# Performance work log

Measured on AMD Instinct MI355X. Metric: run time of the kernel, lower is better.

## Reference

```python
import jax, jax.numpy as jnp
import numpy as np

INPUT_SIZE = 1024
HIDDEN_SIZE = 2048
BATCH = 8192


def setup_inputs() -> dict:
    key = jax.random.key(0)
    k1, k2, k3, k4, k5 = jax.random.split(key, 5)
    input_tensor = jax.random.normal(k1, (BATCH, INPUT_SIZE), dtype=jnp.float32)
    h_0 = jax.random.normal(k2, (BATCH, HIDDEN_SIZE), dtype=jnp.float32)
    c_0 = jax.random.normal(k3, (BATCH, HIDDEN_SIZE), dtype=jnp.float32)
    # parameters: weight [input_size, 3*hidden], weight_hidden [hidden, 3*hidden], bias [3*hidden]
    weight = jax.random.normal(k4, (INPUT_SIZE, 3 * HIDDEN_SIZE), dtype=jnp.float32) * 0.02
    weight_hidden = jax.random.normal(k5, (HIDDEN_SIZE, 3 * HIDDEN_SIZE), dtype=jnp.float32) * 0.02
    bias = jnp.zeros((3 * HIDDEN_SIZE,), dtype=jnp.float32)
    return {
        "input_tensor": input_tensor,
        "h_0": h_0,
        "c_0": c_0,
        "weight": weight,
        "weight_hidden": weight_hidden,
        "bias": bias,
    }


def reference(input_tensor, h_0, c_0, weight, weight_hidden, bias):
    hidden_size = h_0.shape[-1]
    # pre-activations: x @ W + h_0 @ W_h + b  -> [batch, 3*hidden]
    gates = input_tensor @ weight + h_0 @ weight_hidden + bias
    f, i, c = jnp.split(gates, 3, axis=1)
    # c_1 = sigmoid(f) * c_0 + sigmoid(i) * tanh(c)
    c_1 = jax.nn.sigmoid(f) * c_0 + jax.nn.sigmoid(i) * jnp.tanh(c)
    return c_1
```

## Files before the change

kernel.cpp:

```cpp
#include <hip/hip_runtime.h>
#include <stdint.h>


#define BATCH 8192
#define INSZ  1024
#define HID   2048
#define NG    6144
#define KTOT  3072
#define KTILES 96

typedef __attribute__((ext_vector_type(8))) short short8;
typedef __attribute__((ext_vector_type(4))) short short4v;
typedef __attribute__((ext_vector_type(4))) float f32x4;
typedef __attribute__((ext_vector_type(4))) unsigned short u16x4;

__device__ __forceinline__ unsigned short f32_to_bf16(float f) {
  uint32_t u = __builtin_bit_cast(uint32_t, f);
  u += 0x7fffu + ((u >> 16) & 1u);
  return (unsigned short)(u >> 16);
}

#define PACKA_BLOCKS 24576
#define PACKB_BLOCKS 18432
__global__ __launch_bounds__(256) void pack_ab_kernel(
    const float* __restrict__ x, const float* __restrict__ h,
    const float* __restrict__ W, const float* __restrict__ Wh,
    unsigned short* __restrict__ Ap, unsigned short* __restrict__ Bp) {
  if (blockIdx.x < PACKA_BLOCKS) {
    uint32_t q   = blockIdx.x * 256u + threadIdx.x;
    uint32_t kk4 = q & 7u;
    uint32_t m   = (q >> 3) & 8191u;
    uint32_t kt  = q >> 16;
    uint32_t k   = kt * 32u + kk4 * 4u;
    const float* src = (k < INSZ) ? (x + (size_t)m * INSZ + k)
                                  : (h + (size_t)m * HID + (k - INSZ));
    float4 v = *(const float4*)src;
    u16x4 o;
    o.x = f32_to_bf16(v.x); o.y = f32_to_bf16(v.y);
    o.z = f32_to_bf16(v.z); o.w = f32_to_bf16(v.w);
    uint32_t c  = kk4 >> 1, hh = kk4 & 1;
    uint32_t sm = (m + (m >> 2)) & 3u;
    *(u16x4*)(Ap + ((size_t)kt * BATCH + m) * 32 + ((c ^ sm) * 8 + hh * 4)) = o;
  } else {
    uint32_t q  = (blockIdx.x - PACKA_BLOCKS) * 256u + threadIdx.x;
    uint32_t hh = q & 7u;
    uint32_t r  = q >> 3;
    uint32_t n  = r % 6144u;
    uint32_t kt = r / 6144u;
    uint32_t k0 = kt * 32u + hh * 4u;
    float v[4];
#pragma unroll
    for (int t = 0; t < 4; ++t) {
      uint32_t k = k0 + t;
      v[t] = (k < INSZ) ? W[(size_t)k * NG + n]
                        : Wh[(size_t)(k - INSZ) * NG + n];
    }
    u16x4 o;
    o.x = f32_to_bf16(v[0]); o.y = f32_to_bf16(v[1]);
    o.z = f32_to_bf16(v[2]); o.w = f32_to_bf16(v[3]);
    *(u16x4*)(Bp + ((size_t)kt * NG + n) * 32 + hh * 4) = o;
  }
}

__device__ __forceinline__ void lstm_epilogue(
    const f32x4 acc[4][6], int m0, int j0, int wm, int wn, int quad, int l16,
    const float* __restrict__ bias, const float* __restrict__ c0,
    float* __restrict__ out) {
#pragma unroll
  for (int mi = 0; mi < 4; ++mi) {
    int rowb = m0 + wm * 64 + mi * 16 + quad * 4;
#pragma unroll
    for (int p = 0; p < 2; ++p) {
      int j = j0 + (2 * wn + p) * 16 + l16;
      float bfv = bias[j], biv = bias[HID + j], bcv = bias[2 * HID + j];
#pragma unroll
      for (int r = 0; r < 4; ++r) {
        size_t idx = (size_t)(rowb + r) * HID + j;
        float fg = acc[mi][0 + p][r] + bfv;
        float ig = acc[mi][2 + p][r] + biv;
        float cg = acc[mi][4 + p][r] + bcv;
        float sf = 1.f / (1.f + __expf(-fg));
        float si = 1.f / (1.f + __expf(-ig));
        float th = 2.f / (1.f + __expf(-2.f * cg)) - 1.f;
        out[idx] = sf * c0[idx] + si * th;
      }
    }
  }
}

__global__ __launch_bounds__(256, 2) void gemm_packed_kernel(
    const unsigned short* __restrict__ Ap, const unsigned short* __restrict__ Bp,
    const float* __restrict__ bias, const float* __restrict__ c0,
    float* __restrict__ out) {
  __shared__ __align__(16) unsigned short As[2][128 * 32];
  const int tid = threadIdx.x;
  const int lane = tid & 63, w = tid >> 6;
  const int wm = w >> 1, wn = w & 1;
  const int quad = lane >> 4, l16 = lane & 15;
  const int bx = blockIdx.x;
  const int mt = bx & 63, jt = bx >> 6;
  const int m0 = mt * 128, j0 = jt * 64;
  const int sw = (l16 + (l16 >> 2)) & 3;

  f32x4 acc[4][6];
#pragma unroll
  for (int a = 0; a < 4; ++a)
#pragma unroll
    for (int b = 0; b < 6; ++b) acc[a][b] = (f32x4){0.f, 0.f, 0.f, 0.f};

  const unsigned short* bb =
      Bp + ((size_t)(j0 + 2 * wn * 16 + l16)) * 32 + quad * 8;

#define STAGE_A(ktile, buf)                                                    \
  {                                                                            \
    const unsigned short* ga = Ap + ((size_t)(ktile) * BATCH + m0) * 32;       \
    _Pragma("unroll")                                                          \
    for (int i = 0; i < 2; ++i) {                                              \
      int t2 = w * 2 + i;                                                      \
      __builtin_amdgcn_global_load_lds(                                        \
          (__attribute__((address_space(1))) void*)(void*)(ga + t2 * 512 +     \
                                                           lane * 8),          \
          (__attribute__((address_space(3))) void*)(&As[(buf)][0] + t2 * 512), \
          16, 0, 0);                                                           \
    }                                                                          \
  }

#define LOAD_B(ktile, idx)                                                     \
  {                                                                            \
    const unsigned short* bn = bb + (size_t)(ktile) * ((size_t)NG * 32);       \
    _Pragma("unroll")                                                          \
    for (int g = 0; g < 3; ++g)                                                \
      _Pragma("unroll")                                                        \
      for (int p = 0; p < 2; ++p)                                              \
        bf[(idx)][g * 2 + p] = *(const short8*)(bn + g * (HID * 32) + p * 512);\
  }

  short8 bf[2][6];
  STAGE_A(0, 0);
  LOAD_B(0, 0);
  __syncthreads();

#pragma unroll 2
  for (int kt = 0; kt < KTILES; ++kt) {
    const int cur = kt & 1;
    int ktn = kt + 1; if (ktn >= KTILES) ktn = KTILES - 1;
    STAGE_A(ktn, cur ^ 1);
    LOAD_B(ktn, cur ^ 1);
    short8 af[4];
#pragma unroll
    for (int mi = 0; mi < 4; ++mi)
      af[mi] = *(const short8*)(
          &As[cur][0] + (wm * 64 + mi * 16 + l16) * 32 + ((quad ^ sw) * 8));
    __builtin_amdgcn_s_setprio(1);
#pragma unroll
    for (int mi = 0; mi < 4; ++mi)
#pragma unroll
      for (int f = 0; f < 6; ++f)
        acc[mi][f] =
            __builtin_amdgcn_mfma_f32_16x16x32_bf16(af[mi], bf[cur][f], acc[mi][f], 0, 0, 0);
    __builtin_amdgcn_s_setprio(0);
    __syncthreads();
  }
#undef STAGE_A
#undef LOAD_B
  lstm_epilogue(acc, m0, j0, wm, wn, quad, l16, bias, c0, out);
}

__global__ __launch_bounds__(256) void gemm_f32_kernel(
    const float* __restrict__ x, const float* __restrict__ h,
    const float* __restrict__ W, const float* __restrict__ Wh,
    const float* __restrict__ bias, const float* __restrict__ c0,
    float* __restrict__ out) {
  __shared__ __align__(16) unsigned short As[128 * 36];
  __shared__ __align__(16) unsigned short Bs[192 * 36];
  const int tid = threadIdx.x;
  const int lane = tid & 63, w = tid >> 6;
  const int wm = w >> 1, wn = w & 1;
  const int quad = lane >> 4, l16 = lane & 15;
  const int bx = blockIdx.x;
  const int jt = bx & 31, mt = bx >> 5;
  const int m0 = mt * 128, j0 = jt * 64;

  f32x4 acc[4][6];
#pragma unroll
  for (int a = 0; a < 4; ++a)
#pragma unroll
    for (int b = 0; b < 6; ++b) acc[a][b] = (f32x4){0.f, 0.f, 0.f, 0.f};

  for (int kt = 0; kt < KTILES; ++kt) {
    int k0 = kt * 32;
#pragma unroll
    for (int i = 0; i < 4; ++i) {
      int q = i * 256 + tid;
      int m = q >> 3, kk = (q & 7) * 4;
      int k = k0 + kk;
      const float* src = (k < INSZ) ? (x + (size_t)(m0 + m) * INSZ + k)
                                    : (h + (size_t)(m0 + m) * HID + (k - INSZ));
      float4 v = *(const float4*)src;
      u16x4 o;
      o.x = f32_to_bf16(v.x); o.y = f32_to_bf16(v.y);
      o.z = f32_to_bf16(v.z); o.w = f32_to_bf16(v.w);
      *(u16x4*)(As + m * 36 + kk) = o;
    }
#pragma unroll
    for (int i = 0; i < 6; ++i) {
      int q = i * 256 + tid;
      int n = q % 192, kq = (q / 192) * 4;
      int col = (n >> 6) * HID + j0 + (n & 63);
      float vv[4];
#pragma unroll
      for (int t = 0; t < 4; ++t) {
        int k = k0 + kq + t;
        vv[t] = (k < INSZ) ? W[(size_t)k * NG + col]
                           : Wh[(size_t)(k - INSZ) * NG + col];
      }
      u16x4 o;
      o.x = f32_to_bf16(vv[0]); o.y = f32_to_bf16(vv[1]);
      o.z = f32_to_bf16(vv[2]); o.w = f32_to_bf16(vv[3]);
      *(u16x4*)(Bs + n * 36 + kq) = o;
    }
    __syncthreads();
    short8 af[4], bf[6];
#pragma unroll
    for (int mi = 0; mi < 4; ++mi) {
      int base = (wm * 64 + mi * 16 + l16) * 36 + quad * 8;
      short4v lo = *(const short4v*)(As + base);
      short4v hi = *(const short4v*)(As + base + 4);
      af[mi] = __builtin_shufflevector(lo, hi, 0, 1, 2, 3, 4, 5, 6, 7);
    }
#pragma unroll
    for (int g = 0; g < 3; ++g)
#pragma unroll
      for (int p = 0; p < 2; ++p) {
        int base = (g * 64 + (2 * wn + p) * 16 + l16) * 36 + quad * 8;
        short4v lo = *(const short4v*)(Bs + base);
        short4v hi = *(const short4v*)(Bs + base + 4);
        bf[g * 2 + p] = __builtin_shufflevector(lo, hi, 0, 1, 2, 3, 4, 5, 6, 7);
      }
#pragma unroll
    for (int mi = 0; mi < 4; ++mi)
#pragma unroll
      for (int f = 0; f < 6; ++f)
        acc[mi][f] =
            __builtin_amdgcn_mfma_f32_16x16x32_bf16(af[mi], bf[f], acc[mi][f], 0, 0, 0);
    __syncthreads();
  }
  lstm_epilogue(acc, m0, j0, wm, wn, quad, l16, bias, c0, out);
}

extern "C" void kernel_launch(void* const* d_in, const int* in_sizes, int n_in,
                              void* d_out, int out_size, void* d_ws, size_t ws_size,
                              hipStream_t stream) {
  const float* x    = (const float*)d_in[0];
  const float* h0   = (const float*)d_in[1];
  const float* c0   = (const float*)d_in[2];
  const float* W    = (const float*)d_in[3];
  const float* Wh   = (const float*)d_in[4];
  const float* bias = (const float*)d_in[5];
  float* out = (float*)d_out;

  const size_t needA = (size_t)KTOT * BATCH * 2;
  const size_t needB = (size_t)KTOT * NG * 2;
  if (ws_size >= needA + needB) {
    unsigned short* Ap = (unsigned short*)d_ws;
    unsigned short* Bp = Ap + (size_t)KTOT * BATCH;
    pack_ab_kernel<<<PACKA_BLOCKS + PACKB_BLOCKS, 256, 0, stream>>>(x, h0, W, Wh, Ap, Bp);
    gemm_packed_kernel<<<2048, 256, 0, stream>>>(Ap, Bp, bias, c0, out);
  } else {
    gemm_f32_kernel<<<2048, 256, 0, stream>>>(x, h0, W, Wh, bias, c0, out);
  }
}
```

Baseline: 569.4 us.

## Deepen A-tile LDS pipeline to four buffers, one barrier per two k-tiles

The LDS staging buffer for A grows from two to four slots. The main loop now processes two k-tiles per iteration, prefetching A tiles two steps ahead and alternating the B register buffers. This halves the number of workgroup barriers and gives the asynchronous global-to-LDS loads more time to land before they are consumed. In exchange, LDS use per block doubles, and the B loads in registers still have only a one-tile lead.

```diff
diff --git a/kernel.cpp b/kernel.cpp
--- a/kernel.cpp
+++ b/kernel.cpp
@@ -92,7 +92,7 @@
     const unsigned short* __restrict__ Ap, const unsigned short* __restrict__ Bp,
     const float* __restrict__ bias, const float* __restrict__ c0,
     float* __restrict__ out) {
-  __shared__ __align__(16) unsigned short As[2][128 * 32];
+  __shared__ __align__(16) unsigned short As[4][128 * 32];
   const int tid = threadIdx.x;
   const int lane = tid & 63, w = tid >> 6;
   const int wm = w >> 1, wn = w & 1;
@@ -135,34 +135,45 @@
         bf[(idx)][g * 2 + p] = *(const short8*)(bn + g * (HID * 32) + p * 512);\
   }
 
+#define COMPUTE_TILE(buf, bidx)                                                \
+  {                                                                            \
+    short8 af[4];                                                              \
+    _Pragma("unroll")                                                          \
+    for (int mi = 0; mi < 4; ++mi)         \
+      af[mi] = *(const short8*)(                                               \
+          &As[(buf)][0] + (wm * 64 + mi * 16 + l16) * 32 + ((quad ^ sw) * 8)); \
+    __builtin_amdgcn_s_setprio(1);                                             \
+    _Pragma("unroll")                                                          \
+    for (int mi = 0; mi < 4; ++mi)                                             \
+      _Pragma("unroll")                                                        \
+      for (int f = 0; f < 6; ++f)                                              \
+        acc[mi][f] = __builtin_amdgcn_mfma_f32_16x16x32_bf16(                  \
+            af[mi], bf[(bidx)][f], acc[mi][f], 0, 0, 0);                       \
+    __builtin_amdgcn_s_setprio(0);                                             \
+  }
+
   short8 bf[2][6];
   STAGE_A(0, 0);
+  STAGE_A(1, 1);
   LOAD_B(0, 0);
   __syncthreads();
 
-#pragma unroll 2
-  for (int kt = 0; kt < KTILES; ++kt) {
-    const int cur = kt & 1;
-    int ktn = kt + 1; if (ktn >= KTILES) ktn = KTILES - 1;
-    STAGE_A(ktn, cur ^ 1);
-    LOAD_B(ktn, cur ^ 1);
-    short8 af[4];
-#pragma unroll
-    for (int mi = 0; mi < 4; ++mi)
-      af[mi] = *(const short8*)(
-          &As[cur][0] + (wm * 64 + mi * 16 + l16) * 32 + ((quad ^ sw) * 8));
-    __builtin_amdgcn_s_setprio(1);
-#pragma unroll
-    for (int mi = 0; mi < 4; ++mi)
-#pragma unroll
-      for (int f = 0; f < 6; ++f)
-        acc[mi][f] =
-            __builtin_amdgcn_mfma_f32_16x16x32_bf16(af[mi], bf[cur][f], acc[mi][f], 0, 0, 0);
-    __builtin_amdgcn_s_setprio(0);
+  for (int i = 0; i < KTILES / 2; ++i) {
+    const int kt = 2 * i;
+    int s0 = kt + 2; if (s0 >= KTILES) s0 = KTILES - 1;
+    int s1 = kt + 3; if (s1 >= KTILES) s1 = KTILES - 1;
+    STAGE_A(s0, (kt + 2) & 3);
+    STAGE_A(s1, (kt + 3) & 3);
+    LOAD_B(kt + 1, 1);
+    COMPUTE_TILE(kt & 3, 0);
+    int kb2 = kt + 2; if (kb2 >= KTILES) kb2 = KTILES - 1;
+    LOAD_B(kb2, 0);
+    COMPUTE_TILE((kt + 1) & 3, 1);
     __syncthreads();
   }
 #undef STAGE_A
 #undef LOAD_B
+#undef COMPUTE_TILE
   lstm_epilogue(acc, m0, j0, wm, wn, quad, l16, bias, c0, out);
 }
 
```

Result: slower. 584.3 us (+2.6%).
